# Optimization experiments

Measured on AMD Instinct MI355X. Metric: run time of the kernel, lower is better.

The kernel has to match this reference:

```python
import jax, jax.numpy as jnp
import numpy as np

N, K = 50000, 16
IN_FEATS, HIDDEN, T2V = 128, 128, 64


def time2vec(t, w0, b0, W, B):
    # t: [..., 1] -> [..., T2V]; linear term + sin periodic terms
    lin = t * w0 + b0                      # [..., 1]
    per = jnp.sin(t * W + B)               # [..., T2V-1]
    return jnp.concatenate([lin, per], axis=-1)


def setup_inputs() -> dict:
    key = jax.random.key(0)
    ks = jax.random.split(key, 12)
    s = 0.05
    return {
        "x": jax.random.normal(ks[0], (N, IN_FEATS), jnp.float32),
        "ts": jax.random.uniform(ks[1], (N, K), jnp.float32),
        "idx": jax.random.randint(ks[2], (N, K), 0, N),
        "t2v_w0": jax.random.normal(ks[3], (1,), jnp.float32),
        "t2v_b0": jax.random.normal(ks[4], (1,), jnp.float32),
        "t2v_W": jax.random.normal(ks[5], (T2V - 1,), jnp.float32),
        "t2v_B": jax.random.normal(ks[6], (T2V - 1,), jnp.float32),
        "Wq": jax.random.normal(ks[7], (IN_FEATS + T2V, HIDDEN), jnp.float32) * s,
        "Wk": jax.random.normal(ks[8], (IN_FEATS + T2V, HIDDEN), jnp.float32) * s,
        "Wv": jax.random.normal(ks[9], (IN_FEATS + T2V, HIDDEN), jnp.float32) * s,
        "Wo": jax.random.normal(ks[10], (HIDDEN, HIDDEN), jnp.float32) * s,
        "bo": jnp.zeros((HIDDEN,), jnp.float32),
    }


def reference(x, ts, idx, t2v_w0, t2v_b0, t2v_W, t2v_B, Wq, Wk, Wv, Wo, bo):
    # Self representation: node feats + time2vec of zero time offset
    te_self = time2vec(jnp.zeros((x.shape[0], 1), x.dtype), t2v_w0, t2v_b0, t2v_W, t2v_B)  # [N, T2V]
    h_self = jnp.concatenate([x, te_self], axis=-1)           # [N, IN+T2V]

    # Neighbor gather + time2vec of interaction times
    x_nbr = x[idx]                                             # [N, K, IN]
    te_nbr = time2vec(ts[..., None], t2v_w0, t2v_b0, t2v_W, t2v_B)  # [N, K, T2V]
    h_nbr = jnp.concatenate([x_nbr, te_nbr], axis=-1)          # [N, K, IN+T2V]

    # Single-head scaled dot-product attention over neighbors
    q = h_self @ Wq                                            # [N, H]
    k = jnp.einsum('nkf,fh->nkh', h_nbr, Wk)                   # [N, K, H]
    v = jnp.einsum('nkf,fh->nkh', h_nbr, Wv)                   # [N, K, H]
    scores = jnp.einsum('nh,nkh->nk', q, k) / jnp.sqrt(jnp.asarray(HIDDEN, x.dtype))
    attn = jax.nn.softmax(scores, axis=-1)                     # [N, K]
    agg = jnp.einsum('nk,nkh->nh', attn, v)                    # [N, H]

    return jax.nn.relu(agg @ Wo + bo)                          # [N, H]
```

## Files before the change

kernel.cpp:

```cpp
#include <hip/hip_runtime.h>
#include <math.h>

#define NN 50000
#define SCL 0.08838834764831845f

#define QC    0
#define CQK   128
#define WT    192
#define BT    256
#define UBASE 320
#define QXB   0
#define KXB   6400000
#define VOB   12800000
#define QKXB  19200000
#define WCAT  22400000
#define WVOP  22457344

typedef __attribute__((ext_vector_type(8))) short bf16x8;
typedef __attribute__((ext_vector_type(4))) float f32x4;

__device__ __forceinline__ float bfl(unsigned int u) {
  union { unsigned int i; float f; } v; v.i = u << 16; return v.f;
}
__device__ __forceinline__ float bfh(unsigned int u) {
  union { unsigned int i; float f; } v; v.i = u & 0xffff0000u; return v.f;
}
__device__ __forceinline__ unsigned short f2bf(float f) {
  union { float f; unsigned int i; } v; v.f = f;
  return (unsigned short)((v.i + 0x7fff + ((v.i >> 16) & 1)) >> 16);
}

__global__ __launch_bounds__(128) void tgat_prep(
    const float* __restrict__ Wq, const float* __restrict__ Wk,
    const float* __restrict__ Wv, const float* __restrict__ Wo,
    const float* __restrict__ t2v_w0, const float* __restrict__ t2v_b0,
    const float* __restrict__ t2v_W, const float* __restrict__ t2v_B,
    float* __restrict__ ws, unsigned short* __restrict__ ub) {
  const int h = threadIdx.x;
  const int b = blockIdx.x;
  __shared__ float row_s[128];

  if (b < 128) {
    const float* wvrow = Wv + b * 128;
    float acc = 0.f;
#pragma unroll 8
    for (int f = 0; f < 128; ++f) acc += wvrow[f] * Wo[f * 128 + h];
    ub[WCAT + (256 + h) * 128 + b] = f2bf(acc);
  } else if (b < 192) {
    const int j = b - 128;
    const float* wvrow = Wv + (128 + j) * 128;
    float acc = 0.f;
#pragma unroll 8
    for (int f = 0; f < 128; ++f) acc += wvrow[f] * Wo[f * 128 + h];
    row_s[h] = acc;
    __syncthreads();
    if (h < 64) {
      unsigned* wp = (unsigned*)(ub + WVOP);
      wp[j * 64 + h] = (unsigned)f2bf(row_s[2 * h]) |
                       ((unsigned)f2bf(row_s[2 * h + 1]) << 16);
    }
  } else if (b == 192) {
    float acc = t2v_b0[0] * Wq[128 * 128 + h];
    for (int j = 1; j < 64; ++j)
      acc += __sinf(t2v_B[j - 1]) * Wq[(128 + j) * 128 + h];
    ws[QC + h] = acc;
  } else if (b < 321) {
    const int f = b - 193;
    if (h < 64) {
      const float* wqrow = Wq + f * 128;
      const float* wkrow = Wk + (128 + h) * 128;
      float acc = 0.f;
#pragma unroll 8
      for (int i = 0; i < 128; ++i) acc += wqrow[i] * wkrow[i];
      ub[WCAT + (384 + h) * 128 + f] = f2bf(SCL * acc);
    }
  } else if (b < 577) {
    const int c = b - 321;
    const float v = (c < 128) ? Wq[h * 128 + c] : Wk[h * 128 + (c - 128)];
    ub[WCAT + c * 128 + h] = f2bf(v);
  } else {
    if (h < 64) {
      ws[WT + h] = (h == 0) ? t2v_w0[0] : t2v_W[h - 1];
      ws[BT + h] = (h == 0) ? t2v_b0[0] : t2v_B[h - 1];
    }
  }
}

__global__ __launch_bounds__(64) void tgat_prep2(
    const float* __restrict__ Wk, float* __restrict__ ws) {
  const int j = threadIdx.x;
  const float* wkrow = Wk + (128 + j) * 128;
  float acc = 0.f;
#pragma unroll 8
  for (int i = 0; i < 128; ++i) acc += ws[QC + i] * wkrow[i];
  ws[CQK + j] = SCL * acc;
}

__global__ __launch_bounds__(256) void tgat_precomp_mfma(
    const float* __restrict__ x, float* ws) {
  const int lane = threadIdx.x & 63;
  const int wv = threadIdx.x >> 6;
  const int mr = blockIdx.x * 16;
  unsigned short* ub = (unsigned short*)(ws + UBASE);
  const unsigned short* wc = ub + WCAT;
  const int arow = lane & 15;
  const int ko = (lane >> 4) * 8;
  const int rbase = (lane >> 4) * 4;

  bf16x8 afr[4];
  {
    const float* xrow = x + (size_t)(mr + arow) * 128;
#pragma unroll
    for (int kk = 0; kk < 4; ++kk) {
      const float4 lo = *(const float4*)(xrow + kk * 32 + ko);
      const float4 hi = *(const float4*)(xrow + kk * 32 + ko + 4);
      bf16x8 f;
      f[0] = (short)f2bf(lo.x); f[1] = (short)f2bf(lo.y);
      f[2] = (short)f2bf(lo.z); f[3] = (short)f2bf(lo.w);
      f[4] = (short)f2bf(hi.x); f[5] = (short)f2bf(hi.y);
      f[6] = (short)f2bf(hi.z); f[7] = (short)f2bf(hi.w);
      afr[kk] = f;
    }
  }

  unsigned short* qxb  = ub + QXB;
  unsigned short* kxb  = ub + KXB;
  unsigned short* vob  = ub + VOB;
  unsigned short* qkxb = ub + QKXB;

#pragma unroll
  for (int c7 = 0; c7 < 7; ++c7) {
    const int ct = wv * 7 + c7;
    const int col = ct * 16 + arow;
    bf16x8 bfr[4];
#pragma unroll
    for (int kk = 0; kk < 4; ++kk)
      bfr[kk] = *(const bf16x8*)(wc + (size_t)col * 128 + kk * 32 + ko);
    f32x4 acc = {0.f, 0.f, 0.f, 0.f};
#pragma unroll
    for (int kk = 0; kk < 4; ++kk)
      acc = __builtin_amdgcn_mfma_f32_16x16x32_bf16(afr[kk], bfr[kk], acc, 0, 0, 0);

    const int gc = ct * 16 + arow;
    if (ct < 8) {
      const float qc = ws[QC + gc];
#pragma unroll
      for (int r = 0; r < 4; ++r)
        qxb[(size_t)(mr + rbase + r) * 128 + gc] = f2bf((acc[r] + qc) * SCL);
    } else if (ct < 16) {
#pragma unroll
      for (int r = 0; r < 4; ++r)
        kxb[(size_t)(mr + rbase + r) * 128 + (gc - 128)] = f2bf(acc[r]);
    } else if (ct < 24) {
#pragma unroll
      for (int r = 0; r < 4; ++r)
        vob[(size_t)(mr + rbase + r) * 128 + (gc - 256)] = f2bf(acc[r]);
    } else {
      const float cq = ws[CQK + gc - 384];
#pragma unroll
      for (int r = 0; r < 4; ++r)
        qkxb[(size_t)(mr + rbase + r) * 64 + (gc - 384)] = f2bf(acc[r] + cq);
    }
  }
}

__global__ __launch_bounds__(256, 6) void tgat_main(
    const float* __restrict__ ts, const int* __restrict__ idx,
    const float* __restrict__ bo, const float* __restrict__ ws,
    float* __restrict__ out) {
  const int lane = threadIdx.x & 63;
  const int wv   = threadIdx.x >> 6;
  const int my_k = lane >> 2, my_c = lane & 3;

  __shared__ float lds[4 * 1312];
  float* te_s = lds + wv * 1312;
  float* s_s  = te_s + 1088;
  float* q_s  = te_s + 1104;
  float* qk_s = te_s + 1248;

  const unsigned short* ubr = (const unsigned short*)(ws + UBASE);
  const unsigned short* qxb  = ubr + QXB;
  const unsigned short* kxb  = ubr + KXB;
  const unsigned short* vob  = ubr + VOB;
  const unsigned short* qkxb = ubr + QKXB;
  const unsigned* wvp = (const unsigned*)(ubr + WVOP);

  const int n = blockIdx.x * 4 + wv;

  const int   iv = idx[n * 16 + (lane & 15)];
  const float tv = ts[n * 16 + (lane & 15)];
  const unsigned qu = ((const unsigned*)(qxb + (size_t)n * 128))[lane];
  unsigned qku = 0;
  if (lane < 32) qku = ((const unsigned*)(qkxb + (size_t)n * 64))[lane];
  const float2 bo2 = ((const float2*)bo)[lane];

  const int i_myk = __shfl(iv, my_k, 64);
  const unsigned short* kr = kxb + (size_t)i_myk * 128 + my_c * 32;
  const uint4 kx0 = *(const uint4*)(kr);
  const uint4 kx1 = *(const uint4*)(kr + 8);
  const uint4 kx2 = *(const uint4*)(kr + 16);
  const uint4 kx3 = *(const uint4*)(kr + 24);
  unsigned int vg[16];
#pragma unroll
  for (int k = 0; k < 16; ++k) {
    const int ik = __shfl(iv, k, 64);
    vg[k] = ((const unsigned int*)(vob + (size_t)ik * 128))[lane];
  }

  const float tvk = __shfl(tv, my_k, 64);
  float te[16];
  {
    const float4* w4 = (const float4*)(ws + WT + my_c * 16);
    const float4* b4 = (const float4*)(ws + BT + my_c * 16);
#pragma unroll
    for (int i4 = 0; i4 < 4; ++i4) {
      const float4 a = w4[i4], b = b4[i4];
      te[i4*4+0] = __sinf(tvk * a.x + b.x);
      te[i4*4+1] = __sinf(tvk * a.y + b.y);
      te[i4*4+2] = __sinf(tvk * a.z + b.z);
      te[i4*4+3] = __sinf(tvk * a.w + b.w);
    }
  }
  if (my_c == 0) te[0] = tvk * (ws[WT]) + ws[BT];

  {
    const int f = 2 * lane;
    const int qi = (f >> 5) * 36 + (f & 31);
    q_s[qi] = bfl(qu); q_s[qi + 1] = bfh(qu);
  }
  if (lane < 32) { qk_s[2 * lane] = bfl(qku); qk_s[2 * lane + 1] = bfh(qku); }
#pragma unroll
  for (int i = 0; i < 16; ++i)
    te_s[(my_c * 16 + i) * 17 + my_k] = te[i];
  asm volatile("s_waitcnt lgkmcnt(0)" ::: "memory");

  float p = 0.f;
  {
    const float4* qb = (const float4*)(q_s + my_c * 36);
#pragma unroll
    for (int q8 = 0; q8 < 4; ++q8) {
      const uint4 u = (q8 == 0) ? kx0 : (q8 == 1) ? kx1 : (q8 == 2) ? kx2 : kx3;
      const float4 qlo = qb[q8 * 2], qhi = qb[q8 * 2 + 1];
      p += bfl(u.x) * qlo.x + bfh(u.x) * qlo.y;
      p += bfl(u.y) * qlo.z + bfh(u.y) * qlo.w;
      p += bfl(u.z) * qhi.x + bfh(u.z) * qhi.y;
      p += bfl(u.w) * qhi.z + bfh(u.w) * qhi.w;
    }
    const float4* qq4 = (const float4*)(qk_s + my_c * 16);
#pragma unroll
    for (int i4 = 0; i4 < 4; ++i4) {
      const float4 q = qq4[i4];
      p += te[i4*4+0]*q.x + te[i4*4+1]*q.y + te[i4*4+2]*q.z + te[i4*4+3]*q.w;
    }
  }
  p += __shfl_xor(p, 1, 64);
  p += __shfl_xor(p, 2, 64);
  if (my_c == 0) s_s[my_k] = p;
  asm volatile("s_waitcnt lgkmcnt(0)" ::: "memory");

  float a[16];
  {
    float sv[16];
    const float4* s4 = (const float4*)s_s;
#pragma unroll
    for (int i4 = 0; i4 < 4; ++i4) {
      const float4 v = s4[i4];
      sv[i4*4+0]=v.x; sv[i4*4+1]=v.y; sv[i4*4+2]=v.z; sv[i4*4+3]=v.w;
    }
    float m = sv[0];
#pragma unroll
    for (int k = 1; k < 16; ++k) m = fmaxf(m, sv[k]);
    float sum = 0.f;
#pragma unroll
    for (int k = 0; k < 16; ++k) { a[k] = __expf(sv[k] - m); sum += a[k]; }
    const float inv = 1.f / sum;
#pragma unroll
    for (int k = 0; k < 16; ++k) a[k] *= inv;
  }

  {
    float ta = 0.f;
#pragma unroll
    for (int k = 0; k < 16; ++k) ta += a[k] * te_s[lane * 17 + k];
    qk_s[lane] = ta;
  }
  asm volatile("s_waitcnt lgkmcnt(0)" ::: "memory");

  float acc0 = bo2.x, acc1 = bo2.y;
#pragma unroll
  for (int k = 0; k < 16; ++k) {
    const unsigned int u = vg[k];
    acc0 += a[k] * bfl(u);
    acc1 += a[k] * bfh(u);
  }

  {
    const float4* ta4 = (const float4*)qk_s;
#pragma unroll
    for (int j4 = 0; j4 < 16; ++j4) {
      const float4 tb = ta4[j4];
      const unsigned u0 = wvp[(j4*4+0) * 64 + lane];
      const unsigned u1 = wvp[(j4*4+1) * 64 + lane];
      const unsigned u2 = wvp[(j4*4+2) * 64 + lane];
      const unsigned u3 = wvp[(j4*4+3) * 64 + lane];
      acc0 += tb.x * bfl(u0); acc1 += tb.x * bfh(u0);
      acc0 += tb.y * bfl(u1); acc1 += tb.y * bfh(u1);
      acc0 += tb.z * bfl(u2); acc1 += tb.z * bfh(u2);
      acc0 += tb.w * bfl(u3); acc1 += tb.w * bfh(u3);
    }
  }

  float2 o; o.x = fmaxf(acc0, 0.f); o.y = fmaxf(acc1, 0.f);
  ((float2*)(out + (size_t)n * 128))[lane] = o;
}

extern "C" void kernel_launch(void* const* d_in, const int* in_sizes, int n_in,
                              void* d_out, int out_size, void* d_ws, size_t ws_size,
                              hipStream_t stream) {
  const float* x    = (const float*)d_in[0];
  const float* ts   = (const float*)d_in[1];
  const int*   idx  = (const int*)  d_in[2];
  const float* w0   = (const float*)d_in[3];
  const float* b0   = (const float*)d_in[4];
  const float* t2vW = (const float*)d_in[5];
  const float* t2vB = (const float*)d_in[6];
  const float* Wq   = (const float*)d_in[7];
  const float* Wk   = (const float*)d_in[8];
  const float* Wv   = (const float*)d_in[9];
  const float* Wo   = (const float*)d_in[10];
  const float* bo   = (const float*)d_in[11];
  float* ws = (float*)d_ws;
  unsigned short* ub = (unsigned short*)(ws + UBASE);
  float* out = (float*)d_out;

  tgat_prep<<<578, 128, 0, stream>>>(Wq, Wk, Wv, Wo, w0, b0, t2vW, t2vB, ws, ub);
  tgat_prep2<<<1, 64, 0, stream>>>(Wk, ws);
  tgat_precomp_mfma<<<3125, 256, 0, stream>>>(x, ws);
  tgat_main<<<12500, 256, 0, stream>>>(ts, idx, bo, ws, out);
}
```

Before: 234.8 us.

## Fold prep2 into prep, shrink precompute blocks, stage WVO table in LDS

```diff
diff --git a/kernel.cpp b/kernel.cpp
--- a/kernel.cpp
+++ b/kernel.cpp
@@ -39,6 +39,7 @@
   const int h = threadIdx.x;
   const int b = blockIdx.x;
   __shared__ float row_s[128];
+  __shared__ float sm_s[64];
 
   if (b < 128) {
     const float* wvrow = Wv + b * 128;
@@ -78,28 +79,34 @@
     const int c = b - 321;
     const float v = (c < 128) ? Wq[h * 128 + c] : Wk[h * 128 + (c - 128)];
     ub[WCAT + c * 128 + h] = f2bf(v);
-  } else {
+  } else if (b == 577) {
     if (h < 64) {
       ws[WT + h] = (h == 0) ? t2v_w0[0] : t2v_W[h - 1];
       ws[BT + h] = (h == 0) ? t2v_b0[0] : t2v_B[h - 1];
     }
-  }
-}
-
-__global__ __launch_bounds__(64) void tgat_prep2(
-    const float* __restrict__ Wk, float* __restrict__ ws) {
-  const int j = threadIdx.x;
-  const float* wkrow = Wk + (128 + j) * 128;
-  float acc = 0.f;
-#pragma unroll 8
-  for (int i = 0; i < 128; ++i) acc += ws[QC + i] * wkrow[i];
-  ws[CQK + j] = SCL * acc;
-}
-
-__global__ __launch_bounds__(256) void tgat_precomp_mfma(
+  } else {
+    if (h < 64)
+      sm_s[h] = (h == 0) ? t2v_b0[0] : __sinf(t2v_B[h - 1]);
+    __syncthreads();
+    float qc = 0.f;
+#pragma unroll 8
+    for (int m = 0; m < 64; ++m)
+      qc += sm_s[m] * Wq[(128 + m) * 128 + h];
+    row_s[h] = qc;
+    __syncthreads();
+    if (h < 64) {
+      const float* wkrow = Wk + (128 + h) * 128;
+      float acc = 0.f;
+#pragma unroll 8
+      for (int i = 0; i < 128; ++i) acc += row_s[i] * wkrow[i];
+      ws[CQK + h] = SCL * acc;
+    }
+  }
+}
+
+__global__ __launch_bounds__(64) void tgat_precomp_mfma(
     const float* __restrict__ x, float* ws) {
-  const int lane = threadIdx.x & 63;
-  const int wv = threadIdx.x >> 6;
+  const int lane = threadIdx.x;
   const int mr = blockIdx.x * 16;
   unsigned short* ub = (unsigned short*)(ws + UBASE);
   const unsigned short* wc = ub + WCAT;
@@ -128,9 +135,8 @@
   unsigned short* vob  = ub + VOB;
   unsigned short* qkxb = ub + QKXB;
 
-#pragma unroll
-  for (int c7 = 0; c7 < 7; ++c7) {
-    const int ct = wv * 7 + c7;
+#pragma unroll 4
+  for (int ct = 0; ct < 28; ++ct) {
     const int col = ct * 16 + arow;
     bf16x8 bfr[4];
 #pragma unroll
@@ -164,7 +170,7 @@
   }
 }
 
-__global__ __launch_bounds__(256, 6) void tgat_main(
+__global__ __launch_bounds__(256, 4) void tgat_main(
     const float* __restrict__ ts, const int* __restrict__ idx,
     const float* __restrict__ bo, const float* __restrict__ ws,
     float* __restrict__ out) {
@@ -173,6 +179,7 @@
   const int my_k = lane >> 2, my_c = lane & 3;
 
   __shared__ float lds[4 * 1312];
+  __shared__ unsigned wvo_l[4096];
   float* te_s = lds + wv * 1312;
   float* s_s  = te_s + 1088;
   float* q_s  = te_s + 1104;
@@ -183,9 +190,15 @@
   const unsigned short* kxb  = ubr + KXB;
   const unsigned short* vob  = ubr + VOB;
   const unsigned short* qkxb = ubr + QKXB;
-  const unsigned* wvp = (const unsigned*)(ubr + WVOP);
 
   const int n = blockIdx.x * 4 + wv;
+
+  {
+    const uint4* wvp = (const uint4*)(ubr + WVOP);
+#pragma unroll
+    for (int i = 0; i < 4; ++i)
+      ((uint4*)wvo_l)[threadIdx.x + i * 256] = wvp[threadIdx.x + i * 256];
+  }
 
   const int   iv = idx[n * 16 + (lane & 15)];
   const float tv = ts[n * 16 + (lane & 15)];
@@ -294,15 +307,16 @@
     acc1 += a[k] * bfh(u);
   }
 
+  __syncthreads();
   {
     const float4* ta4 = (const float4*)qk_s;
 #pragma unroll
     for (int j4 = 0; j4 < 16; ++j4) {
       const float4 tb = ta4[j4];
-      const unsigned u0 = wvp[(j4*4+0) * 64 + lane];
-      const unsigned u1 = wvp[(j4*4+1) * 64 + lane];
-      const unsigned u2 = wvp[(j4*4+2) * 64 + lane];
-      const unsigned u3 = wvp[(j4*4+3) * 64 + lane];
+      const unsigned u0 = wvo_l[(j4*4+0) * 64 + lane];
+      const unsigned u1 = wvo_l[(j4*4+1) * 64 + lane];
+      const unsigned u2 = wvo_l[(j4*4+2) * 64 + lane];
+      const unsigned u3 = wvo_l[(j4*4+3) * 64 + lane];
       acc0 += tb.x * bfl(u0); acc1 += tb.x * bfh(u0);
       acc0 += tb.y * bfl(u1); acc1 += tb.y * bfh(u1);
       acc0 += tb.z * bfl(u2); acc1 += tb.z * bfh(u2);
@@ -333,8 +347,7 @@
   unsigned short* ub = (unsigned short*)(ws + UBASE);
   float* out = (float*)d_out;
 
-  tgat_prep<<<578, 128, 0, stream>>>(Wq, Wk, Wv, Wo, w0, b0, t2vW, t2vB, ws, ub);
-  tgat_prep2<<<1, 64, 0, stream>>>(Wk, ws);
-  tgat_precomp_mfma<<<3125, 256, 0, stream>>>(x, ws);
+  tgat_prep<<<579, 128, 0, stream>>>(Wq, Wk, Wv, Wo, w0, b0, t2vW, t2vB, ws, ub);
+  tgat_precomp_mfma<<<3125, 64, 0, stream>>>(x, ws);
   tgat_main<<<12500, 256, 0, stream>>>(ts, idx, bo, ws, out);
 }
```

Measured after the change: 215.2 us. -8.3%, faster.
